# Optimization experiments

Hardware: AMD Instinct MI355X
Metric: run time of the kernel (lower is better)

## Reference

```python
import jax, jax.numpy as jnp
import numpy as np

MAX_COC = 50.0
NUM_PLANES = 32
KERNEL_CAP = 31
B, C, H, W = 4, 3, 512, 512


def _plane_kernels():
    """Static per-plane Gaussian kernels, mirroring the torch loop exactly."""
    planes = np.linspace(0.0, MAX_COC, NUM_PLANES)
    kernels = []
    for coc in planes:
        if coc < 0.5:
            kernels.append(None)  # identity (no blur)
            continue
        sigma = coc / 2.355
        k = int(2 * coc + 1)
        if k % 2 == 0:
            k += 1
        k = min(k, KERNEL_CAP)
        coords = np.arange(k, dtype=np.float32) - k // 2
        g = np.exp(-coords ** 2 / (2.0 * sigma ** 2)).astype(np.float32)
        g = g / g.sum()
        kernels.append(np.outer(g, g).astype(np.float32))
    return planes, kernels


def _depthwise_blur(x, kern2d):
    # x: [B,C,H,W]; kern2d: [k,k] shared across channels (grouped conv, groups=C)
    c = x.shape[1]
    k = kern2d.shape[0]
    w = jnp.broadcast_to(jnp.asarray(kern2d, dtype=x.dtype)[None, None], (c, 1, k, k))
    return jax.lax.conv_general_dilated(
        x, w, window_strides=(1, 1), padding=[(k // 2, k // 2)] * 2,
        dimension_numbers=('NCHW', 'OIHW', 'NCHW'), feature_group_count=c)


def setup_inputs() -> dict:
    key = jax.random.key(0)
    k1, k2 = jax.random.split(key)
    sharp_image = jax.random.uniform(k1, (B, C, H, W), dtype=jnp.float32)
    # CoC in pixels, spanning the full [0, MAX_COC) range so all 32 bins fire
    coc_map = jax.random.uniform(k2, (B, 1, H, W), dtype=jnp.float32) * MAX_COC
    return {"sharp_image": sharp_image, "coc_map": coc_map}


def reference(sharp_image, coc_map):
    """Spatially-varying defocus blur: per-plane Gaussian blur + hard-binned blend."""
    planes, kernels = _plane_kernels()
    result = jnp.zeros_like(sharp_image)
    for i in range(NUM_PLANES):
        blurred = sharp_image if kernels[i] is None else _depthwise_blur(sharp_image, kernels[i])
        if i == 0:
            w = coc_map <= (planes[0] + planes[1]) / 2
        elif i == NUM_PLANES - 1:
            w = coc_map > (planes[-2] + planes[-1]) / 2
        else:
            lower = (planes[i - 1] + planes[i]) / 2
            upper = (planes[i] + planes[i + 1]) / 2
            w = (coc_map > lower) & (coc_map <= upper)
        # incremental masked blend (same math as stack-then-sum, less memory)
        result = result + blurred * w.astype(sharp_image.dtype)
    return result
```

## Files before the change

kernel.cpp:

```cpp
#include <hip/hip_runtime.h>
#include <math.h>

typedef _Float16 h2_t __attribute__((ext_vector_type(2)));
typedef _Float16 h4_t __attribute__((ext_vector_type(4)));
typedef _Float16 h8_t __attribute__((ext_vector_type(8)));

#define NP 32
#define KC 31
#define HH 512
#define WW 512
#define BB 4
#define CC 3

#define TXO 64
#define TYO 32
#define NT 512
#define TROWS 62
#define TWORDS 48
#define TILEW (TROWS * TWORDS)
#define WSTR 36


__device__ __forceinline__ double plane_of(int i) {
    const double stepd = 50.0 / 31.0;
    return (i < 31) ? (double)i * stepd : 50.0;
}

__launch_bounds__(512, 2)
__global__ void defocus_kernel(const float* __restrict__ img,
                               const float* __restrict__ coc,
                               float* __restrict__ out) {
    const int tx = threadIdx.x;
    const int ty = threadIdx.y;
    const int tid = ty * 16 + tx;
    const int tilex = blockIdx.x * TXO;
    const int tiley = blockIdx.y * TYO;
    const int b = blockIdx.z;

    __shared__ __align__(16) h2_t wtab[NP * WSTR];
    __shared__ __align__(16) h2_t tile[3 * TILEW];

    const int yo = tiley + ty;
    const int xo = tilex + tx * 4;

    const float4 cv = *(const float4*)&coc[((size_t)b * HH + yo) * WW + xo];

    int foff[6]; int fr[6]; bool g0[6], g1[6];
    #pragma unroll
    for (int i = 0; i < 6; ++i) {
        const int f = tid + i * NT;
        const int r = f / TWORDS;
        const int w = f - r * TWORDS;
        const int gy = tiley - 15 + r;
        const int gx = tilex - 15 + 2 * w;
        const bool rowok = (f < TILEW) && ((unsigned)gy < (unsigned)HH);
        g0[i] = rowok && ((unsigned)gx < (unsigned)WW);
        g1[i] = rowok && ((unsigned)(gx + 1) < (unsigned)WW);
        foff[i] = gy * WW + gx;
        fr[i] = f;
    }
    float sv[3][6][2];
    #pragma unroll
    for (int c = 0; c < 3; ++c) {
        const float* src = img + (size_t)(b * CC + c) * HH * WW;
        #pragma unroll
        for (int i = 0; i < 6; ++i) {
            sv[c][i][0] = g0[i] ? src[foff[i]]     : 0.f;
            sv[c][i][1] = g1[i] ? src[foff[i] + 1] : 0.f;
        }
    }

    {
        const int t = tid & 31;
        #pragma unroll
        for (int pass = 0; pass < 2; ++pass) {
            const int p = (tid >> 5) + 16 * pass;
            const double stepd = 50.0 / 31.0;
            double cocp = (p < 31) ? (double)p * stepd : 50.0;
            float gt;
            if (cocp < 0.5) {
                gt = (t == 15) ? 1.f : 0.f;
            } else {
                double sigma = cocp / 2.355;
                int k = (int)(2.0 * cocp + 1.0);
                if ((k & 1) == 0) k += 1;
                if (k > KC) k = KC;
                int h = k / 2;
                int d = t - 15;
                float denom = (float)(2.0 * sigma * sigma);
                float v = (d >= -h && d <= h && t < KC) ? expf(-(float)(d * d) / denom) : 0.f;
                float s = v;
                #pragma unroll
                for (int off = 1; off < 32; off <<= 1) s += __shfl_xor(s, off, 32);
                gt = v / s;
            }
            const int m = t & 15;
            const int s0 = (t < 16) ? (2 * m) : ((2 * m - 1 < 0) ? 0 : 2 * m - 1);
            const int s1 = (t < 16) ? (2 * m + 1) : (2 * m);
            float w0 = __shfl(gt, s0, 32);
            float w1 = __shfl(gt, s1, 32);
            if (t >= 16 && (2 * m - 1) < 0) w0 = 0.f;
            h2_t w; w.x = (_Float16)w0; w.y = (_Float16)w1;
            wtab[p * WSTR + t] = w;
            if (t < WSTR - 32) {
                h2_t z; z.x = (_Float16)0.f; z.y = (_Float16)0.f;
                wtab[p * WSTR + 32 + t] = z;
            }
        }
    }

    #pragma unroll
    for (int c = 0; c < 3; ++c) {
        #pragma unroll
        for (int i = 0; i < 6; ++i) {
            if (fr[i] < TILEW) {
                h2_t pv; pv.x = (_Float16)sv[c][i][0]; pv.y = (_Float16)sv[c][i][1];
                tile[c * TILEW + fr[i]] = pv;
            }
        }
    }

    const float cocf[4] = {cv.x, cv.y, cv.z, cv.w};
    int idx[4];
    #pragma unroll
    for (int j = 0; j < 4; ++j) {
        const double stepd = 50.0 / 31.0;
        double cd = (double)cocf[j];
        int i0 = (int)floor(cd / stepd + 0.5);
        i0 = min(max(i0, 0), 31);
        if (i0 > 0 && cd <= 0.5 * (plane_of(i0 - 1) + plane_of(i0))) {
            i0 -= 1;
        } else if (i0 < 31 && cd > 0.5 * (plane_of(i0) + plane_of(i0 + 1))) {
            i0 += 1;
        }
        idx[j] = i0;
    }

    __syncthreads();

    h2_t wj[4][16];
    #pragma unroll
    for (int j = 0; j < 4; ++j) {
        const h2_t* wp = &wtab[idx[j] * WSTR + (j & 1) * 16];
        #pragma unroll
        for (int m = 0; m < 4; ++m) {
            h8_t v = *(const h8_t*)(wp + 4 * m);
            #pragma unroll
            for (int q = 0; q < 4; ++q) {
                h2_t t2; t2.x = v[2 * q]; t2.y = v[2 * q + 1];
                wj[j][4 * m + q] = t2;
            }
        }
    }

    #pragma unroll 1
    for (int c = 0; c < 3; ++c) {
        float acc0 = 0.f, acc1 = 0.f, acc2 = 0.f, acc3 = 0.f;
        const h2_t* rowbase = &tile[c * TILEW + ty * TWORDS + 2 * tx];
        #pragma unroll
        for (int dy = 0; dy < KC; ++dy) {
            const h2_t* rp = rowbase + dy * TWORDS;
            h2_t rw[18];
            #pragma unroll
            for (int m = 0; m < 9; ++m) {
                h4_t q = *(const h4_t*)(rp + 2 * m);
                h2_t lo; lo.x = q[0]; lo.y = q[1];
                h2_t hi; hi.x = q[2]; hi.y = q[3];
                rw[2 * m]     = lo;
                rw[2 * m + 1] = hi;
            }
            float rs0 = 0.f, rs1 = 0.f, rs2 = 0.f, rs3 = 0.f;
            #pragma unroll
            for (int m = 0; m < 16; ++m) {
                rs0 = __builtin_amdgcn_fdot2(wj[0][m], rw[m],     rs0, false);
                rs1 = __builtin_amdgcn_fdot2(wj[1][m], rw[m],     rs1, false);
                rs2 = __builtin_amdgcn_fdot2(wj[2][m], rw[m + 1], rs2, false);
                rs3 = __builtin_amdgcn_fdot2(wj[3][m], rw[m + 1], rs3, false);
            }
            float cw0, cw1, cw2, cw3;
            if ((dy & 1) == 0) {
                cw0 = (float)wj[0][dy >> 1].x;
                cw2 = (float)wj[2][dy >> 1].x;
                cw1 = (float)wj[1][dy >> 1].y;
                cw3 = (float)wj[3][dy >> 1].y;
            } else {
                cw0 = (float)wj[0][dy >> 1].y;
                cw2 = (float)wj[2][dy >> 1].y;
                cw1 = (float)wj[1][(dy + 1) >> 1].x;
                cw3 = (float)wj[3][(dy + 1) >> 1].x;
            }
            acc0 += cw0 * rs0;
            acc1 += cw1 * rs1;
            acc2 += cw2 * rs2;
            acc3 += cw3 * rs3;
        }

        *(float4*)&out[((size_t)(b * CC + c) * HH + yo) * WW + xo] =
            make_float4(acc0, acc1, acc2, acc3);
    }
}

extern "C" void kernel_launch(void* const* d_in, const int* in_sizes, int n_in,
                              void* d_out, int out_size, void* d_ws, size_t ws_size,
                              hipStream_t stream) {
    const float* sharp = (const float*)d_in[0];
    const float* cocm  = (const float*)d_in[1];
    float* out = (float*)d_out;

    dim3 grid(WW / TXO, HH / TYO, BB);
    dim3 block(16, 32, 1);
    defocus_kernel<<<grid, block, 0, stream>>>(sharp, cocm, out);
}
```

Measured before the change: 136.8 us.

## Prefetch next channel's tile during current channel's convolution

Instead of loading all three channels into registers up front, only channel 0 is staged before compute. The loads for each following channel are issued at the start of the current channel's convolution loop and written to shared memory afterward, with a barrier after each write. This cuts live registers, from 36 staging floats down to 12, and hides global load latency behind compute. In exchange it adds two block-wide barriers and recomputes the staging addresses for each channel.

```diff
diff --git a/kernel.cpp b/kernel.cpp
--- a/kernel.cpp
+++ b/kernel.cpp
@@ -24,6 +24,19 @@
 __device__ __forceinline__ double plane_of(int i) {
     const double stepd = 50.0 / 31.0;
     return (i < 31) ? (double)i * stepd : 50.0;
+}
+
+__device__ __forceinline__ void stage_addr(int tid, int i, int tiley, int tilex,
+                                           int& off, bool& ok0, bool& ok1) {
+    const int f = tid + i * NT;
+    const int r = f / TWORDS;
+    const int w = f - r * TWORDS;
+    const int gy = tiley - 15 + r;
+    const int gx = tilex - 15 + 2 * w;
+    const bool rowok = (f < TILEW) && ((unsigned)gy < (unsigned)HH);
+    ok0 = rowok && ((unsigned)gx < (unsigned)WW);
+    ok1 = rowok && ((unsigned)(gx + 1) < (unsigned)WW);
+    off = gy * WW + gx;
 }
 
 __launch_bounds__(512, 2)
@@ -45,28 +58,15 @@
 
     const float4 cv = *(const float4*)&coc[((size_t)b * HH + yo) * WW + xo];
 
-    int foff[6]; int fr[6]; bool g0[6], g1[6];
-    #pragma unroll
-    for (int i = 0; i < 6; ++i) {
-        const int f = tid + i * NT;
-        const int r = f / TWORDS;
-        const int w = f - r * TWORDS;
-        const int gy = tiley - 15 + r;
-        const int gx = tilex - 15 + 2 * w;
-        const bool rowok = (f < TILEW) && ((unsigned)gy < (unsigned)HH);
-        g0[i] = rowok && ((unsigned)gx < (unsigned)WW);
-        g1[i] = rowok && ((unsigned)(gx + 1) < (unsigned)WW);
-        foff[i] = gy * WW + gx;
-        fr[i] = f;
-    }
-    float sv[3][6][2];
-    #pragma unroll
-    for (int c = 0; c < 3; ++c) {
-        const float* src = img + (size_t)(b * CC + c) * HH * WW;
+    float s0v[6], s1v[6];
+    {
+        const float* src0 = img + (size_t)(b * CC) * HH * WW;
         #pragma unroll
         for (int i = 0; i < 6; ++i) {
-            sv[c][i][0] = g0[i] ? src[foff[i]]     : 0.f;
-            sv[c][i][1] = g1[i] ? src[foff[i] + 1] : 0.f;
+            int off; bool ok0, ok1;
+            stage_addr(tid, i, tiley, tilex, off, ok0, ok1);
+            s0v[i] = ok0 ? src0[off]     : 0.f;
+            s1v[i] = ok1 ? src0[off + 1] : 0.f;
         }
     }
 
@@ -109,17 +109,6 @@
         }
     }
 
-    #pragma unroll
-    for (int c = 0; c < 3; ++c) {
-        #pragma unroll
-        for (int i = 0; i < 6; ++i) {
-            if (fr[i] < TILEW) {
-                h2_t pv; pv.x = (_Float16)sv[c][i][0]; pv.y = (_Float16)sv[c][i][1];
-                tile[c * TILEW + fr[i]] = pv;
-            }
-        }
-    }
-
     const float cocf[4] = {cv.x, cv.y, cv.z, cv.w};
     int idx[4];
     #pragma unroll
@@ -136,6 +125,15 @@
         idx[j] = i0;
     }
 
+    #pragma unroll
+    for (int i = 0; i < 6; ++i) {
+        const int f = tid + i * NT;
+        if (f < TILEW) {
+            h2_t pv; pv.x = (_Float16)s0v[i]; pv.y = (_Float16)s1v[i];
+            tile[f] = pv;
+        }
+    }
+
     __syncthreads();
 
     h2_t wj[4][16];
@@ -154,7 +152,19 @@
     }
 
     #pragma unroll 1
-    for (int c = 0; c < 3; ++c) {
+    for (int c = 0; c < CC; ++c) {
+        float n0[6], n1[6];
+        if (c + 1 < CC) {
+            const float* srcn = img + (size_t)(b * CC + c + 1) * HH * WW;
+            #pragma unroll
+            for (int i = 0; i < 6; ++i) {
+                int off; bool ok0, ok1;
+                stage_addr(tid, i, tiley, tilex, off, ok0, ok1);
+                n0[i] = ok0 ? srcn[off]     : 0.f;
+                n1[i] = ok1 ? srcn[off + 1] : 0.f;
+            }
+        }
+
         float acc0 = 0.f, acc1 = 0.f, acc2 = 0.f, acc3 = 0.f;
         const h2_t* rowbase = &tile[c * TILEW + ty * TWORDS + 2 * tx];
         #pragma unroll
@@ -197,6 +207,18 @@
 
         *(float4*)&out[((size_t)(b * CC + c) * HH + yo) * WW + xo] =
             make_float4(acc0, acc1, acc2, acc3);
+
+        if (c + 1 < CC) {
+            #pragma unroll
+            for (int i = 0; i < 6; ++i) {
+                const int f = tid + i * NT;
+                if (f < TILEW) {
+                    h2_t pv; pv.x = (_Float16)n0[i]; pv.y = (_Float16)n1[i];
+                    tile[(c + 1) * TILEW + f] = pv;
+                }
+            }
+            __syncthreads();
+        }
     }
 }
 
```

Result: slower. 149.8 us (+9.5%).

## Stage image channels via async global-to-LDS loads overlapped with convolution

Applied to the files above, without the earlier changes.

Replaces the upfront register loads of all three channels with `global_load_lds` transfers into an fp32 LDS staging buffer, one channel at a time. Each staged channel is converted to fp16 in the tile. The next channel's load is issued before the current channel's convolution, so fetching overlaps compute, and register pressure from holding all 36 loaded values drops. The cost is about 24 KB of extra LDS per block, two extra barriers per channel, and extra loads for clamped halo rows.

```diff
diff --git a/kernel.cpp b/kernel.cpp
--- a/kernel.cpp
+++ b/kernel.cpp
@@ -4,6 +4,7 @@
 typedef _Float16 h2_t __attribute__((ext_vector_type(2)));
 typedef _Float16 h4_t __attribute__((ext_vector_type(4)));
 typedef _Float16 h8_t __attribute__((ext_vector_type(8)));
+typedef float    f2_t __attribute__((ext_vector_type(2)));
 
 #define NP 32
 #define KC 31
@@ -19,11 +20,52 @@
 #define TWORDS 48
 #define TILEW (TROWS * TWORDS)
 #define WSTR 36
+#define FSTR 96
+#define FROWS 64
+#define FBUFW (FROWS * FSTR)
 
 
 __device__ __forceinline__ double plane_of(int i) {
     const double stepd = 50.0 / 31.0;
     return (i < 31) ? (double)i * stepd : 50.0;
+}
+
+__device__ __forceinline__ void issue_stage(const float* __restrict__ src,
+                                            float* fbuf, int tid,
+                                            int tiley, int tilex) {
+    #pragma unroll
+    for (int i = 0; i < 12; ++i) {
+        const int f = tid + i * NT;
+        const int r = f / FSTR;
+        const int w = f - r * FSTR;
+        int gy = tiley - 15 + r;  gy = min(max(gy, 0), HH - 1);
+        int gx = tilex - 15 + w;  gx = min(max(gx, 0), WW - 1);
+        const float* gp = src + gy * WW + gx;
+        __builtin_amdgcn_global_load_lds(
+            (const __attribute__((address_space(1))) unsigned int*)gp,
+            (__attribute__((address_space(3))) unsigned int*)(fbuf + f),
+            4, 0, 0);
+    }
+}
+
+__device__ __forceinline__ void convert_tile(const float* fbuf, h2_t* tdst,
+                                             int tid, int tiley, int tilex) {
+    #pragma unroll
+    for (int i = 0; i < 6; ++i) {
+        const int t = tid + i * NT;
+        if (t < TILEW) {
+            const int r = t / TWORDS;
+            const int w = t - r * TWORDS;
+            const int gy = tiley - 15 + r;
+            const int gx = tilex - 15 + 2 * w;
+            const bool rowok = (unsigned)gy < (unsigned)HH;
+            f2_t v = *(const f2_t*)(fbuf + r * FSTR + 2 * w);
+            float v0 = (rowok && (unsigned)gx       < (unsigned)WW) ? v[0] : 0.f;
+            float v1 = (rowok && (unsigned)(gx + 1) < (unsigned)WW) ? v[1] : 0.f;
+            h2_t pv; pv.x = (_Float16)v0; pv.y = (_Float16)v1;
+            tdst[t] = pv;
+        }
+    }
 }
 
 __launch_bounds__(512, 2)
@@ -37,38 +79,16 @@
     const int tiley = blockIdx.y * TYO;
     const int b = blockIdx.z;
 
-    __shared__ __align__(16) h2_t wtab[NP * WSTR];
-    __shared__ __align__(16) h2_t tile[3 * TILEW];
+    __shared__ __align__(16) h2_t  wtab[NP * WSTR];
+    __shared__ __align__(16) h2_t  tile[3 * TILEW];
+    __shared__ __align__(16) float fbuf[FBUFW];
 
     const int yo = tiley + ty;
     const int xo = tilex + tx * 4;
 
     const float4 cv = *(const float4*)&coc[((size_t)b * HH + yo) * WW + xo];
 
-    int foff[6]; int fr[6]; bool g0[6], g1[6];
-    #pragma unroll
-    for (int i = 0; i < 6; ++i) {
-        const int f = tid + i * NT;
-        const int r = f / TWORDS;
-        const int w = f - r * TWORDS;
-        const int gy = tiley - 15 + r;
-        const int gx = tilex - 15 + 2 * w;
-        const bool rowok = (f < TILEW) && ((unsigned)gy < (unsigned)HH);
-        g0[i] = rowok && ((unsigned)gx < (unsigned)WW);
-        g1[i] = rowok && ((unsigned)(gx + 1) < (unsigned)WW);
-        foff[i] = gy * WW + gx;
-        fr[i] = f;
-    }
-    float sv[3][6][2];
-    #pragma unroll
-    for (int c = 0; c < 3; ++c) {
-        const float* src = img + (size_t)(b * CC + c) * HH * WW;
-        #pragma unroll
-        for (int i = 0; i < 6; ++i) {
-            sv[c][i][0] = g0[i] ? src[foff[i]]     : 0.f;
-            sv[c][i][1] = g1[i] ? src[foff[i] + 1] : 0.f;
-        }
-    }
+    issue_stage(img + (size_t)(b * CC) * HH * WW, fbuf, tid, tiley, tilex);
 
     {
         const int t = tid & 31;
@@ -109,17 +129,6 @@
         }
     }
 
-    #pragma unroll
-    for (int c = 0; c < 3; ++c) {
-        #pragma unroll
-        for (int i = 0; i < 6; ++i) {
-            if (fr[i] < TILEW) {
-                h2_t pv; pv.x = (_Float16)sv[c][i][0]; pv.y = (_Float16)sv[c][i][1];
-                tile[c * TILEW + fr[i]] = pv;
-            }
-        }
-    }
-
     const float cocf[4] = {cv.x, cv.y, cv.z, cv.w};
     int idx[4];
     #pragma unroll
@@ -138,6 +147,10 @@
 
     __syncthreads();
 
+    convert_tile(fbuf, tile, tid, tiley, tilex);
+
+    __syncthreads();
+
     h2_t wj[4][16];
     #pragma unroll
     for (int j = 0; j < 4; ++j) {
@@ -154,7 +167,11 @@
     }
 
     #pragma unroll 1
-    for (int c = 0; c < 3; ++c) {
+    for (int c = 0; c < CC; ++c) {
+        if (c + 1 < CC)
+            issue_stage(img + (size_t)(b * CC + c + 1) * HH * WW, fbuf,
+                        tid, tiley, tilex);
+
         float acc0 = 0.f, acc1 = 0.f, acc2 = 0.f, acc3 = 0.f;
         const h2_t* rowbase = &tile[c * TILEW + ty * TWORDS + 2 * tx];
         #pragma unroll
@@ -197,6 +214,12 @@
 
         *(float4*)&out[((size_t)(b * CC + c) * HH + yo) * WW + xo] =
             make_float4(acc0, acc1, acc2, acc3);
+
+        if (c + 1 < CC) {
+            __syncthreads();
+            convert_tile(fbuf, tile + (c + 1) * TILEW, tid, tiley, tilex);
+            __syncthreads();
+        }
     }
 }
 
```

Measured after the change: 169.7 us. 24.1% more time.
